# Kernel tuning notes

Hardware: AMD Instinct MI355X
Metric: run time of the kernel (lower is better)

The kernel has to match this reference:

```python
import jax, jax.numpy as jnp
import numpy as np

B, C, H, W = 4, 256, 64, 64
CH = C // 2  # inner channels


def setup_inputs() -> dict:
    key = jax.random.key(0)
    ks = jax.random.split(key, 9)
    s_in = 1.0 / np.sqrt(C)
    s_w = 1.0 / np.sqrt(CH)
    return {
        "x": jax.random.normal(ks[0], (B, C, H, W), dtype=jnp.float32),
        "theta_w": jax.random.normal(ks[1], (CH, C), dtype=jnp.float32) * s_in,
        "theta_b": jax.random.normal(ks[2], (CH,), dtype=jnp.float32) * s_in,
        "phi_w": jax.random.normal(ks[3], (CH, C), dtype=jnp.float32) * s_in,
        "phi_b": jax.random.normal(ks[4], (CH,), dtype=jnp.float32) * s_in,
        "g_w": jax.random.normal(ks[5], (CH, C), dtype=jnp.float32) * s_in,
        "g_b": jax.random.normal(ks[6], (CH,), dtype=jnp.float32) * s_in,
        "W_w": jax.random.normal(ks[7], (C, CH), dtype=jnp.float32) * s_w,
        "W_b": jax.random.normal(ks[8], (C,), dtype=jnp.float32) * s_w,
    }


def _proj(x_flat, w, b):
    # 1x1 conv == channel matmul; x_flat: [B, C, N] -> [B, O, N]
    return jnp.einsum("oc,bcn->bon", w, x_flat) + b[None, :, None]


def reference(x, theta_w, theta_b, phi_w, phi_b, g_w, g_b, W_w, W_b):
    b, c, h, w = x.shape
    n = h * w
    xf = x.reshape(b, c, n)
    theta = _proj(xf, theta_w, theta_b)  # [B, CH, N]
    phi = _proj(xf, phi_w, phi_b)        # [B, CH, N]
    g = _proj(xf, g_w, g_b)              # [B, CH, N]
    # scores[b,i,j] = theta[:, :, i] . phi[:, :, j]; softmax over j
    attn = jax.nn.softmax(jnp.einsum("bci,bcj->bij", theta, phi), axis=-1)
    # torch: bmm(g_x, attn) -> out[b,c,i] = sum_j g[b,c,j] * attn[b,j,i]
    out = jnp.einsum("bcj,bji->bci", g, attn)  # [B, CH, N]
    out = jnp.einsum("oc,bcn->bon", W_w, out) + W_b[None, :, None]
    return out.reshape(b, c, h, w) + x
```

## Files before the change

### kernel.cpp

```cpp
#include <hip/hip_runtime.h>
#include <hip/hip_bf16.h>
#include <math.h>

#define BB    4
#define CC    256
#define CHN   128
#define NN    4096

typedef short short8 __attribute__((ext_vector_type(8)));
typedef float f32x4  __attribute__((ext_vector_type(4)));
typedef float f32x16 __attribute__((ext_vector_type(16)));
typedef unsigned short u16;
typedef u16  us4 __attribute__((ext_vector_type(4)));

#define MFMA16(a, b, c) __builtin_amdgcn_mfma_f32_16x16x32_bf16((a), (b), (c), 0, 0, 0)
#define MFMA32(a, b, c) __builtin_amdgcn_mfma_f32_32x32x16_bf16((a), (b), (c), 0, 0, 0)
#define LOG2E 1.4426950408889634f

#if __has_builtin(__builtin_amdgcn_exp2f)
#define EXP2F(x) __builtin_amdgcn_exp2f(x)
#else
#define EXP2F(x) exp2f(x)
#endif
#if __has_builtin(__builtin_amdgcn_logf)
#define LOG2F(x) __builtin_amdgcn_logf(x)
#else
#define LOG2F(x) log2f(x)
#endif

static __device__ __forceinline__ u16 f2bf(float f) {
    union { float f; unsigned u; } v; v.f = f;
    unsigned r = v.u + 0x7FFFu + ((v.u >> 16) & 1u);
    return (u16)(r >> 16);
}
static __device__ __forceinline__ unsigned pkbf(float a, float b) {
    __hip_bfloat162 h = __float22bfloat162_rn(make_float2(a, b));
    return *reinterpret_cast<unsigned*>(&h);
}
static __device__ __forceinline__ int sw128(int row, int u) {
    return row * 128 + ((u ^ (row & 7)) << 3);
}
static __device__ __forceinline__ void gload16(const u16* g, u16* l) {
    __builtin_amdgcn_global_load_lds(
        (const __attribute__((address_space(1))) void*)g,
        (__attribute__((address_space(3))) void*)l, 16, 0, 0);
}

typedef union { unsigned u[4]; short8 v; } bfrag;

#if __has_builtin(__builtin_amdgcn_permlane32_swap)
#define REPACK(sv, f) do { \
    unsigned e0 = pkbf(EXP2F(sv[0]),  EXP2F(sv[1])); \
    unsigned e1 = pkbf(EXP2F(sv[2]),  EXP2F(sv[3])); \
    unsigned e2 = pkbf(EXP2F(sv[4]),  EXP2F(sv[5])); \
    unsigned e3 = pkbf(EXP2F(sv[6]),  EXP2F(sv[7])); \
    unsigned e4 = pkbf(EXP2F(sv[8]),  EXP2F(sv[9])); \
    unsigned e5 = pkbf(EXP2F(sv[10]), EXP2F(sv[11])); \
    unsigned e6 = pkbf(EXP2F(sv[12]), EXP2F(sv[13])); \
    unsigned e7 = pkbf(EXP2F(sv[14]), EXP2F(sv[15])); \
    auto r02 = __builtin_amdgcn_permlane32_swap(e0, e2, false, false); \
    auto r13 = __builtin_amdgcn_permlane32_swap(e1, e3, false, false); \
    auto r46 = __builtin_amdgcn_permlane32_swap(e4, e6, false, false); \
    auto r57 = __builtin_amdgcn_permlane32_swap(e5, e7, false, false); \
    f[0].u[0] = r02[0]; f[0].u[1] = r13[0]; \
    f[0].u[2] = r02[1]; f[0].u[3] = r13[1]; \
    f[1].u[0] = r46[0]; f[1].u[1] = r57[0]; \
    f[1].u[2] = r46[1]; f[1].u[3] = r57[1]; \
} while (0)
#else
#define REPACK(sv, f) do { \
    unsigned e0 = pkbf(EXP2F(sv[0]),  EXP2F(sv[1])); \
    unsigned e1 = pkbf(EXP2F(sv[2]),  EXP2F(sv[3])); \
    unsigned e2 = pkbf(EXP2F(sv[4]),  EXP2F(sv[5])); \
    unsigned e3 = pkbf(EXP2F(sv[6]),  EXP2F(sv[7])); \
    unsigned e4 = pkbf(EXP2F(sv[8]),  EXP2F(sv[9])); \
    unsigned e5 = pkbf(EXP2F(sv[10]), EXP2F(sv[11])); \
    unsigned e6 = pkbf(EXP2F(sv[12]), EXP2F(sv[13])); \
    unsigned e7 = pkbf(EXP2F(sv[14]), EXP2F(sv[15])); \
    unsigned q0 = __shfl_xor(e0, 32), q1 = __shfl_xor(e1, 32); \
    unsigned q2 = __shfl_xor(e2, 32), q3 = __shfl_xor(e3, 32); \
    unsigned q4 = __shfl_xor(e4, 32), q5 = __shfl_xor(e5, 32); \
    unsigned q6 = __shfl_xor(e6, 32), q7 = __shfl_xor(e7, 32); \
    f[0].u[0] = lh ? q2 : e0;  f[0].u[1] = lh ? q3 : e1; \
    f[0].u[2] = lh ? e2 : q0;  f[0].u[3] = lh ? e3 : q1; \
    f[1].u[0] = lh ? q6 : e4;  f[1].u[1] = lh ? q7 : e5; \
    f[1].u[2] = lh ? e6 : q4;  f[1].u[3] = lh ? e7 : q5; \
} while (0)
#endif

__global__ __launch_bounds__(256) void k_cvtw(
    const float* __restrict__ tw, const float* __restrict__ pw,
    const float* __restrict__ gw, const float* __restrict__ Ww,
    u16* __restrict__ wall)
{
    int idx = (blockIdx.x * 256 + threadIdx.x) * 4;
    const float* s = (idx < 32768) ? tw
                   : (idx < 65536) ? pw
                   : (idx < 98304) ? gw : Ww;
    float sc = (idx < 32768) ? LOG2E : 1.0f;
    float4 v = *(const float4*)(s + (idx & 32767));
    us4 r = { f2bf(v.x * sc), f2bf(v.y * sc), f2bf(v.z * sc), f2bf(v.w * sc) };
    *(us4*)(wall + idx) = r;
}

__global__ __launch_bounds__(512) void k_proj(
    const float* __restrict__ x, const u16* __restrict__ wall,
    const float* __restrict__ tb, const float* __restrict__ pb,
    const float* __restrict__ gbias,
    u16* __restrict__ tht, u16* __restrict__ pht, u16* __restrict__ gg)
{
    __shared__ u16 xs[64 * 264];
    __shared__ u16 gbuf[128 * 68];
    const int tid = threadIdx.x;
    const int n0  = blockIdx.x * 64;
    const int b   = blockIdx.y;
    const int ln  = tid & 15, q = (tid >> 4) & 3, wid = tid >> 6;
    const int ow  = wid & 1, nw = wid >> 1;

    for (int p = 0; p < 8; ++p) {
        int id = p * 512 + tid;
        int c = id >> 4, n4 = (id & 15) * 4;
        float4 xv = *(const float4*)(x + ((size_t)b * CC + c) * NN + n0 + n4);
        xs[(n4 + 0) * 264 + c] = f2bf(xv.x);
        xs[(n4 + 1) * 264 + c] = f2bf(xv.y);
        xs[(n4 + 2) * 264 + c] = f2bf(xv.z);
        xs[(n4 + 3) * 264 + c] = f2bf(xv.w);
    }
    __syncthreads();

    short8 bfr[8];
    #pragma unroll
    for (int ks = 0; ks < 8; ++ks)
        bfr[ks] = *(const short8*)(&xs[(nw * 16 + ln) * 264 + ks * 32 + q * 8]);

    for (int pr = 0; pr < 3; ++pr) {
        const u16* wsrc = wall + pr * 32768;
        f32x4 acc[4];
        #pragma unroll
        for (int oo = 0; oo < 4; ++oo) acc[oo] = (f32x4){0.f, 0.f, 0.f, 0.f};
        for (int ks = 0; ks < 8; ++ks) {
            short8 a[4];
            #pragma unroll
            for (int oo = 0; oo < 4; ++oo)
                a[oo] = *(const short8*)(wsrc + (size_t)(ow*64 + oo*16 + ln) * 256 + ks*32 + q*8);
            #pragma unroll
            for (int oo = 0; oo < 4; ++oo)
                acc[oo] = MFMA16(a[oo], bfr[ks], acc[oo]);
        }
        const float* bias = (pr == 0) ? tb : (pr == 1 ? pb : gbias);
        const float bsc = (pr == 0) ? LOG2E : 1.0f;
        if (pr < 2) {
            u16* dst = (pr == 0) ? tht : pht;
            const int n = n0 + nw * 16 + ln;
            #pragma unroll
            for (int oo = 0; oo < 4; ++oo) {
                int o = ow * 64 + oo * 16 + q * 4;
                float4 bv = *(const float4*)(bias + o);
                f32x4 v = acc[oo];
                uint2 r = { pkbf(v.x + bv.x * bsc, v.y + bv.y * bsc),
                            pkbf(v.z + bv.z * bsc, v.w + bv.w * bsc) };
                *(uint2*)(dst + ((size_t)b * NN + n) * CHN + o) = r;
            }
        } else {
            const int nl = nw * 16 + ln;
            #pragma unroll
            for (int oo = 0; oo < 4; ++oo) {
                int o = ow * 64 + oo * 16 + q * 4;
                float4 bv = *(const float4*)(bias + o);
                f32x4 v = acc[oo];
                gbuf[(o + 0) * 68 + nl] = f2bf(v.x + bv.x);
                gbuf[(o + 1) * 68 + nl] = f2bf(v.y + bv.y);
                gbuf[(o + 2) * 68 + nl] = f2bf(v.z + bv.z);
                gbuf[(o + 3) * 68 + nl] = f2bf(v.w + bv.w);
            }
            __syncthreads();
            for (int p = 0; p < 4; ++p) {
                int id = p * 512 + tid;
                int c = id >> 4, n4 = (id & 15) * 4;
                us4 r = *(const us4*)(&gbuf[c * 68 + n4]);
                *(us4*)(gg + ((size_t)b * CHN + c) * NN + n0 + n4) = r;
            }
        }
    }
}

__global__ __launch_bounds__(512, 2) void k_rowsum(
    const u16* __restrict__ tht, const u16* __restrict__ pht,
    float* __restrict__ Z)
{
    __shared__ u16 ph_s[2][128 * 128];
    const int tid = threadIdx.x;
    const int j0  = blockIdx.x * 256;
    const int i00 = blockIdx.y * 1024;
    const int b   = blockIdx.z;
    const int l   = tid & 63, w = tid >> 6;
    const int lm  = l & 31, lh = l >> 5;
    const u16* thb = tht + (size_t)b * NN * CHN;
    const u16* phb = pht + (size_t)b * NN * CHN;

    short8 ar[8];
    #pragma unroll
    for (int ks = 0; ks < 8; ++ks)
        ar[ks] = *(const short8*)(thb + (size_t)(j0 + w*32 + lm) * CHN + ks*16 + lh*8);

    for (int p = 0; p < 4; ++p) {
        int id = p * 512 + tid;
        int row = id >> 4, u = id & 15;
        short8 v = *(const short8*)(phb + (size_t)(i00 + row) * CHN + u * 8);
        *(short8*)(&ph_s[0][sw128(row, u)]) = v;
    }

    float zp[16];
    #pragma unroll
    for (int r = 0; r < 16; ++r) zp[r] = 0.f;

    for (int is = 0; is < 8; ++is) {
        __syncthreads();
        if (is < 7) {
            for (int p = 0; p < 4; ++p) {
                int id = p * 512 + tid;
                int row = id >> 4, u = id & 15;
                short8 v = *(const short8*)(phb + (size_t)(i00 + (is+1)*128 + row) * CHN + u * 8);
                *(short8*)(&ph_s[(is + 1) & 1][sw128(row, u)]) = v;
            }
        }
        const u16* cur = ph_s[is & 1];

        #pragma unroll
        for (int ii = 0; ii < 4; ++ii) {
            f32x16 s;
            #pragma unroll
            for (int r = 0; r < 16; ++r) s[r] = 0.f;
            #pragma unroll
            for (int ks = 0; ks < 8; ++ks) {
                short8 bfrag = *(const short8*)(&cur[sw128(ii*32 + lm, ks*2 + lh)]);
                s = MFMA32(ar[ks], bfrag, s);
            }
            #pragma unroll
            for (int r = 0; r < 16; ++r) zp[r] += EXP2F(s[r]);
        }
    }

    float zr[16];
    #pragma unroll
    for (int r = 0; r < 16; ++r) {
        float v = zp[r];
        v += __shfl_xor(v, 1);
        v += __shfl_xor(v, 2);
        v += __shfl_xor(v, 4);
        v += __shfl_xor(v, 8);
        v += __shfl_xor(v, 16);
        zr[r] = v;
    }
    if (lm == 0) {
        #pragma unroll
        for (int r = 0; r < 16; ++r) {
            int j = j0 + w*32 + (r & 3) + 8*(r >> 2) + 4*lh;
            atomicAdd(&Z[(size_t)b * NN + j], zr[r]);
        }
    }
}

__global__ __launch_bounds__(256) void k_log(
    const float* __restrict__ Z, float* __restrict__ L)
{
    int idx = (blockIdx.x * 256 + threadIdx.x) * 4;
    float4 z = *(const float4*)(Z + idx);
    float4 r = { -LOG2F(z.x), -LOG2F(z.y), -LOG2F(z.z), -LOG2F(z.w) };
    *(float4*)(L + idx) = r;
}

__global__ __launch_bounds__(512) void k_attn(
    const u16* __restrict__ tht, const u16* __restrict__ pht,
    const u16* __restrict__ gg, const float* __restrict__ Lbuf,
    u16* __restrict__ innerT)
{
    __shared__ u16 smem[4][128 * 128];
    const int tid = threadIdx.x;
    const int i0  = blockIdx.x * 256;
    const int jq  = blockIdx.y;
    const int b   = blockIdx.z;
    const int w   = tid >> 6;
    const int iw  = w & 3;
    const int jw  = w >> 2;
    const int lm  = tid & 31, lh = (tid >> 5) & 1;

    const u16*  thb = tht + (size_t)b * NN * CHN;
    const u16*  ggb = gg  + (size_t)b * CHN * NN;
    const float* Lb = Lbuf + (size_t)b * NN;

    int offT[4], offG[4];
    #pragma unroll
    for (int p = 0; p < 4; ++p) {
        int row = p * 32 + (tid >> 4);
        int u   = (tid & 15) ^ (row & 7);
        offT[p] = row * CHN + u * 8;
        offG[p] = row * NN  + u * 8;
    }

    short8 phr[2][8];
    #pragma unroll
    for (int ih = 0; ih < 2; ++ih)
        #pragma unroll
        for (int ks = 0; ks < 8; ++ks)
            phr[ih][ks] = *(const short8*)(pht +
                ((size_t)b * NN + i0 + iw*64 + ih*32 + lm) * CHN + ks*16 + lh*8);

    #pragma unroll
    for (int p = 0; p < 4; ++p) {
        gload16(thb + (size_t)(jq * 1024) * CHN + offT[p], &smem[0][p*4096 + (w << 9)]);
        gload16(ggb + jq * 1024 + offG[p],                 &smem[2][p*4096 + (w << 9)]);
    }
    __syncthreads();

    f32x16 pacc[4][2];
    #pragma unroll
    for (int ct = 0; ct < 4; ++ct)
        #pragma unroll
        for (int ih = 0; ih < 2; ++ih)
            #pragma unroll
            for (int r = 0; r < 16; ++r) pacc[ct][ih][r] = 0.f;

    for (int s = 0; s < 8; ++s) {
        const int j0s = jq * 1024 + s * 128;
        const u16* thc = smem[s & 1];
        const u16* gc  = smem[2 + (s & 1)];

        if (s < 7) {
            const int nb = (s + 1) & 1;
            #pragma unroll
            for (int p = 0; p < 4; ++p) {
                gload16(thb + (size_t)(j0s + 128) * CHN + offT[p], &smem[nb][p*4096 + (w << 9)]);
                gload16(ggb + (j0s + 128) + offG[p],               &smem[2 + nb][p*4096 + (w << 9)]);
            }
        }

        #pragma unroll
        for (int jx = 0; jx < 2; ++jx) {
            const int jj = jw * 2 + jx;
            f32x16 sv0;
            #pragma unroll
            for (int rq = 0; rq < 4; ++rq) {
                float4 Lv = *(const float4*)(Lb + j0s + jj*32 + rq*8 + lh*4);
                sv0[rq*4 + 0] = Lv.x; sv0[rq*4 + 1] = Lv.y;
                sv0[rq*4 + 2] = Lv.z; sv0[rq*4 + 3] = Lv.w;
            }
            f32x16 sv1 = sv0;
            #pragma unroll
            for (int ks = 0; ks < 8; ++ks) {
                short8 a = *(const short8*)(&thc[sw128(jj*32 + lm, ks*2 + lh)]);
                sv0 = MFMA32(a, phr[0][ks], sv0);
                sv1 = MFMA32(a, phr[1][ks], sv1);
            }
            bfrag fA[2], fB[2];
            REPACK(sv0, fA);
            REPACK(sv1, fB);
            #pragma unroll
            for (int h = 0; h < 2; ++h) {
                #pragma unroll
                for (int ct = 0; ct < 4; ++ct) {
                    short8 ag = *(const short8*)(&gc[sw128(ct*32 + lm, jj*4 + h*2 + lh)]);
                    pacc[ct][0] = MFMA32(ag, fA[h].v, pacc[ct][0]);
                    pacc[ct][1] = MFMA32(ag, fB[h].v, pacc[ct][1]);
                }
            }
        }
        __syncthreads();
    }

    float* fb = (float*)smem;
    if (jw == 1) {
        #pragma unroll
        for (int ct = 0; ct < 4; ++ct)
            #pragma unroll
            for (int ih = 0; ih < 2; ++ih) {
                const int il = ih*32 + lm;
                #pragma unroll
                for (int rq = 0; rq < 4; ++rq) {
                    const int c4 = ct*8 + rq*2 + lh;
                    f32x4 v = { pacc[ct][ih][rq*4+0], pacc[ct][ih][rq*4+1],
                                pacc[ct][ih][rq*4+2], pacc[ct][ih][rq*4+3] };
                    *(f32x4*)(fb + iw*8192 + il*128 + ((c4 ^ (il & 7)) << 2)) = v;
                }
            }
    }
    __syncthreads();
    if (jw == 0) {
        u16* dst = innerT + ((size_t)jq * BB + b) * (size_t)NN * CHN;
        #pragma unroll
        for (int ct = 0; ct < 4; ++ct)
            #pragma unroll
            for (int ih = 0; ih < 2; ++ih) {
                const int il = ih*32 + lm;
                const int i  = i0 + iw*64 + il;
                #pragma unroll
                for (int rq = 0; rq < 4; ++rq) {
                    const int c4 = ct*8 + rq*2 + lh;
                    f32x4 v = *(const f32x4*)(fb + iw*8192 + il*128 + ((c4 ^ (il & 7)) << 2));
                    uint2 r = { pkbf(pacc[ct][ih][rq*4+0] + v[0], pacc[ct][ih][rq*4+1] + v[1]),
                                pkbf(pacc[ct][ih][rq*4+2] + v[2], pacc[ct][ih][rq*4+3] + v[3]) };
                    *(uint2*)(dst + (size_t)i * CHN + ct*32 + rq*8 + lh*4) = r;
                }
            }
    }
}

__global__ __launch_bounds__(512, 2) void k_final(
    const u16* __restrict__ innerT, const float* __restrict__ x,
    const u16* __restrict__ Wwbf, const float* __restrict__ Wb,
    float* __restrict__ out)
{
    __shared__ u16 w_s[256 * 128];
    __shared__ u16 a_s[64 * 128];
    const int tid = threadIdx.x;
    const int n0  = blockIdx.x * 64;
    const int b   = blockIdx.y;
    const int l   = tid & 63, w = tid >> 6;
    const int lm  = l & 31, lh = l >> 5;

    for (int p = 0; p < 8; ++p) {
        int id = p * 512 + tid;
        int row = id >> 4, u = id & 15;
        *(short8*)(&w_s[sw128(row, u)]) = *(const short8*)(Wwbf + (size_t)row * CHN + u * 8);
    }
    __syncthreads();

    short8 aw[8];
    #pragma unroll
    for (int ks = 0; ks < 8; ++ks)
        aw[ks] = *(const short8*)(&w_s[sw128(w*32 + lm, ks*2 + lh)]);

    f32x16 acc[2];
    #pragma unroll
    for (int nt = 0; nt < 2; ++nt)
        #pragma unroll
        for (int r = 0; r < 16; ++r) acc[nt][r] = 0.f;

    for (int jq = 0; jq < 4; ++jq) {
        __syncthreads();
        for (int p = 0; p < 2; ++p) {
            int id = p * 512 + tid;
            int row = id >> 4, u = id & 15;
            *(short8*)(&a_s[sw128(row, u)]) =
                *(const short8*)(innerT + (((size_t)jq * BB + b) * NN + n0 + row) * CHN + u * 8);
        }
        __syncthreads();
        #pragma unroll
        for (int ks = 0; ks < 8; ++ks) {
            short8 bn[2];
            #pragma unroll
            for (int nt = 0; nt < 2; ++nt)
                bn[nt] = *(const short8*)(&a_s[sw128(nt*32 + lm, ks*2 + lh)]);
            acc[0] = MFMA32(aw[ks], bn[0], acc[0]);
            acc[1] = MFMA32(aw[ks], bn[1], acc[1]);
        }
    }

    #pragma unroll
    for (int nt = 0; nt < 2; ++nt) {
        const int n = n0 + nt*32 + lm;
        #pragma unroll
        for (int r = 0; r < 16; ++r) {
            const int o = w*32 + (r & 3) + 8*(r >> 2) + 4*lh;
            const size_t idx = ((size_t)b * CC + o) * NN + n;
            out[idx] = acc[nt][r] + Wb[o] + x[idx];
        }
    }
}

extern "C" void kernel_launch(void* const* d_in, const int* in_sizes, int n_in,
                              void* d_out, int out_size, void* d_ws, size_t ws_size,
                              hipStream_t stream)
{
    const float* x  = (const float*)d_in[0];
    const float* tw = (const float*)d_in[1];
    const float* tb = (const float*)d_in[2];
    const float* pw = (const float*)d_in[3];
    const float* pb = (const float*)d_in[4];
    const float* gw = (const float*)d_in[5];
    const float* gb = (const float*)d_in[6];
    const float* Ww = (const float*)d_in[7];
    const float* Wb = (const float*)d_in[8];
    float* out = (float*)d_out;

    char* p = (char*)d_ws;
    const size_t proj_u16 = (size_t)BB * NN * CHN;
    u16*   tht    = (u16*)p;   p += proj_u16 * 2;
    u16*   pht    = (u16*)p;   p += proj_u16 * 2;
    u16*   gg     = (u16*)p;   p += proj_u16 * 2;
    u16*   wall   = (u16*)p;   p += (size_t)131072 * 2;
    float* Z      = (float*)p; p += (size_t)BB * NN * 4;
    float* Lbuf   = (float*)p; p += (size_t)BB * NN * 4;
    u16*   innerT = (u16*)p;

    hipMemsetAsync(Z, 0, (size_t)BB * NN * sizeof(float), stream);
    k_cvtw  <<<128, 256, 0, stream>>>(tw, pw, gw, Ww, wall);
    k_proj  <<<dim3(64, BB), 512, 0, stream>>>(x, wall, tb, pb, gb, tht, pht, gg);
    k_rowsum<<<dim3(16, 4, BB), 512, 0, stream>>>(tht, pht, Z);
    k_log   <<<16, 256, 0, stream>>>(Z, Lbuf);
    k_attn  <<<dim3(16, 4, BB), 512, 0, stream>>>(tht, pht, gg, Lbuf, innerT);
    k_final <<<dim3(64, BB), 512, 0, stream>>>(innerT, x, wall + 98304, Wb, out);
}
```

Baseline: 211.0 us.

## Split attention j-range into 8 chunks with 4-wave blocks, drop in-block reduction

The attention kernel now splits the key dimension into 8 chunks of 512 instead of 4 chunks of 1024 and runs 256-thread blocks. Each wave owns a 64-row i-slice and processes a whole 64-wide j-tile, which removes the shared-memory reduction between two wave groups and its extra barrier. Shared memory per block halves and the grid doubles, which should raise occupancy and parallelism. In exchange the partial-output buffer doubles in size, so the final kernel reads 8 bf16 partials instead of 4 and does more memory traffic.

```diff
diff --git a/kernel.cpp b/kernel.cpp
--- a/kernel.cpp
+++ b/kernel.cpp
@@ -39,6 +39,9 @@
 }
 static __device__ __forceinline__ int sw128(int row, int u) {
     return row * 128 + ((u ^ (row & 7)) << 3);
+}
+static __device__ __forceinline__ int sw64(int row, int u) {
+    return row * 64 + ((u ^ (row & 7)) << 3);
 }
 static __device__ __forceinline__ void gload16(const u16* g, u16* l) {
     __builtin_amdgcn_global_load_lds(
@@ -270,19 +273,18 @@
     *(float4*)(L + idx) = r;
 }
 
-__global__ __launch_bounds__(512) void k_attn(
+__global__ __launch_bounds__(256) void k_attn(
     const u16* __restrict__ tht, const u16* __restrict__ pht,
     const u16* __restrict__ gg, const float* __restrict__ Lbuf,
     u16* __restrict__ innerT)
 {
-    __shared__ u16 smem[4][128 * 128];
+    __shared__ u16 th_s[2][64 * 128];
+    __shared__ u16 g_s [2][128 * 64];
     const int tid = threadIdx.x;
     const int i0  = blockIdx.x * 256;
     const int jq  = blockIdx.y;
     const int b   = blockIdx.z;
     const int w   = tid >> 6;
-    const int iw  = w & 3;
-    const int jw  = w >> 2;
     const int lm  = tid & 31, lh = (tid >> 5) & 1;
 
     const u16*  thb = tht + (size_t)b * NN * CHN;
@@ -292,10 +294,11 @@
     int offT[4], offG[4];
     #pragma unroll
     for (int p = 0; p < 4; ++p) {
-        int row = p * 32 + (tid >> 4);
-        int u   = (tid & 15) ^ (row & 7);
-        offT[p] = row * CHN + u * 8;
-        offG[p] = row * NN  + u * 8;
+        int id = p * 256 + tid;
+        int rT = id >> 4, uT = (id & 15) ^ (rT & 7);
+        offT[p] = rT * CHN + uT * 8;
+        int rG = id >> 3, uG = (id & 7) ^ (rG & 7);
+        offG[p] = rG * NN + uG * 8;
     }
 
     short8 phr[2][8];
@@ -304,12 +307,12 @@
         #pragma unroll
         for (int ks = 0; ks < 8; ++ks)
             phr[ih][ks] = *(const short8*)(pht +
-                ((size_t)b * NN + i0 + iw*64 + ih*32 + lm) * CHN + ks*16 + lh*8);
+                ((size_t)b * NN + i0 + w*64 + ih*32 + lm) * CHN + ks*16 + lh*8);
 
     #pragma unroll
     for (int p = 0; p < 4; ++p) {
-        gload16(thb + (size_t)(jq * 1024) * CHN + offT[p], &smem[0][p*4096 + (w << 9)]);
-        gload16(ggb + jq * 1024 + offG[p],                 &smem[2][p*4096 + (w << 9)]);
+        gload16(thb + (size_t)(jq * 512) * CHN + offT[p], &th_s[0][0] + p*2048 + tid*8);
+        gload16(ggb + jq * 512 + offG[p],                 &g_s [0][0] + p*2048 + tid*8);
     }
     __syncthreads();
 
@@ -322,22 +325,21 @@
             for (int r = 0; r < 16; ++r) pacc[ct][ih][r] = 0.f;
 
     for (int s = 0; s < 8; ++s) {
-        const int j0s = jq * 1024 + s * 128;
-        const u16* thc = smem[s & 1];
-        const u16* gc  = smem[2 + (s & 1)];
+        const int j0s = jq * 512 + s * 64;
+        const u16* thc = th_s[s & 1];
+        const u16* gc  = g_s [s & 1];
 
         if (s < 7) {
             const int nb = (s + 1) & 1;
             #pragma unroll
             for (int p = 0; p < 4; ++p) {
-                gload16(thb + (size_t)(j0s + 128) * CHN + offT[p], &smem[nb][p*4096 + (w << 9)]);
-                gload16(ggb + (j0s + 128) + offG[p],               &smem[2 + nb][p*4096 + (w << 9)]);
-            }
-        }
-
-        #pragma unroll
-        for (int jx = 0; jx < 2; ++jx) {
-            const int jj = jw * 2 + jx;
+                gload16(thb + (size_t)(j0s + 64) * CHN + offT[p], &th_s[nb][0] + p*2048 + tid*8);
+                gload16(ggb + (j0s + 64) + offG[p],               &g_s [nb][0] + p*2048 + tid*8);
+            }
+        }
+
+        #pragma unroll
+        for (int jj = 0; jj < 2; ++jj) {
             f32x16 sv0;
             #pragma unroll
             for (int rq = 0; rq < 4; ++rq) {
@@ -359,7 +361,7 @@
             for (int h = 0; h < 2; ++h) {
                 #pragma unroll
                 for (int ct = 0; ct < 4; ++ct) {
-                    short8 ag = *(const short8*)(&gc[sw128(ct*32 + lm, jj*4 + h*2 + lh)]);
+                    short8 ag = *(const short8*)(&gc[sw64(ct*32 + lm, jj*4 + h*2 + lh)]);
                     pacc[ct][0] = MFMA32(ag, fA[h].v, pacc[ct][0]);
                     pacc[ct][1] = MFMA32(ag, fB[h].v, pacc[ct][1]);
                 }
@@ -368,40 +370,20 @@
         __syncthreads();
     }
 
-    float* fb = (float*)smem;
-    if (jw == 1) {
-        #pragma unroll
-        for (int ct = 0; ct < 4; ++ct)
-            #pragma unroll
-            for (int ih = 0; ih < 2; ++ih) {
-                const int il = ih*32 + lm;
-                #pragma unroll
-                for (int rq = 0; rq < 4; ++rq) {
-                    const int c4 = ct*8 + rq*2 + lh;
-                    f32x4 v = { pacc[ct][ih][rq*4+0], pacc[ct][ih][rq*4+1],
-                                pacc[ct][ih][rq*4+2], pacc[ct][ih][rq*4+3] };
-                    *(f32x4*)(fb + iw*8192 + il*128 + ((c4 ^ (il & 7)) << 2)) = v;
-                }
-            }
-    }
-    __syncthreads();
-    if (jw == 0) {
-        u16* dst = innerT + ((size_t)jq * BB + b) * (size_t)NN * CHN;
-        #pragma unroll
-        for (int ct = 0; ct < 4; ++ct)
-            #pragma unroll
-            for (int ih = 0; ih < 2; ++ih) {
-                const int il = ih*32 + lm;
-                const int i  = i0 + iw*64 + il;
-                #pragma unroll
-                for (int rq = 0; rq < 4; ++rq) {
-                    const int c4 = ct*8 + rq*2 + lh;
-                    f32x4 v = *(const f32x4*)(fb + iw*8192 + il*128 + ((c4 ^ (il & 7)) << 2));
-                    uint2 r = { pkbf(pacc[ct][ih][rq*4+0] + v[0], pacc[ct][ih][rq*4+1] + v[1]),
-                                pkbf(pacc[ct][ih][rq*4+2] + v[2], pacc[ct][ih][rq*4+3] + v[3]) };
-                    *(uint2*)(dst + (size_t)i * CHN + ct*32 + rq*8 + lh*4) = r;
-                }
-            }
+    u16* dst = innerT + ((size_t)jq * BB + b) * (size_t)NN * CHN;
+    #pragma unroll
+    for (int ct = 0; ct < 4; ++ct) {
+        #pragma unroll
+        for (int ih = 0; ih < 2; ++ih) {
+            const int i = i0 + w*64 + ih*32 + lm;
+            #pragma unroll
+            for (int rq = 0; rq < 4; ++rq) {
+                const int c0 = ct*32 + rq*8 + lh*4;
+                uint2 r = { pkbf(pacc[ct][ih][rq*4+0], pacc[ct][ih][rq*4+1]),
+                            pkbf(pacc[ct][ih][rq*4+2], pacc[ct][ih][rq*4+3]) };
+                *(uint2*)(dst + (size_t)i * CHN + c0) = r;
+            }
+        }
     }
 }
 
@@ -436,7 +418,7 @@
         #pragma unroll
         for (int r = 0; r < 16; ++r) acc[nt][r] = 0.f;
 
-    for (int jq = 0; jq < 4; ++jq) {
+    for (int jq = 0; jq < 8; ++jq) {
         __syncthreads();
         for (int p = 0; p < 2; ++p) {
             int id = p * 512 + tid;
@@ -498,6 +480,6 @@
     k_proj  <<<dim3(64, BB), 512, 0, stream>>>(x, wall, tb, pb, gb, tht, pht, gg);
     k_rowsum<<<dim3(16, 4, BB), 512, 0, stream>>>(tht, pht, Z);
     k_log   <<<16, 256, 0, stream>>>(Z, Lbuf);
-    k_attn  <<<dim3(16, 4, BB), 512, 0, stream>>>(tht, pht, gg, Lbuf, innerT);
+    k_attn  <<<dim3(16, 8, BB), 256, 0, stream>>>(tht, pht, gg, Lbuf, innerT);
     k_final <<<dim3(64, BB), 512, 0, stream>>>(innerT, x, wall + 98304, Wb, out);
 }
```

Result: no change. 210.8 us (-0.1%).
